# Kernel optimization log

Measured on AMD Instinct MI355X. Metric: run time of the kernel, lower is better.

## Reference

```python
import jax, jax.numpy as jnp
import numpy as np

B, S, D, H = 2, 2048, 512, 8
DK = D // H

def setup_inputs() -> dict:
    key = jax.random.key(0)
    ks = jax.random.split(key, 13)
    inp = {
        'query': jax.random.normal(ks[0], (B, S, D), jnp.float32),
        'key': jax.random.normal(ks[1], (B, S, D), jnp.float32),
        'value': jax.random.normal(ks[2], (B, S, D), jnp.float32),
        'group_prob': jax.random.uniform(ks[3], (B, S, S), jnp.float32),
        'mask': jax.random.randint(ks[4], (B, S, S), 0, 2, jnp.int32),
        'Wq': jax.random.normal(ks[5], (D, D), jnp.float32) * 0.02,
        'bq': jax.random.normal(ks[6], (D,), jnp.float32) * 0.02,
        'Wk': jax.random.normal(ks[7], (D, D), jnp.float32) * 0.02,
        'bk': jax.random.normal(ks[8], (D,), jnp.float32) * 0.02,
        'Wv': jax.random.normal(ks[9], (D, D), jnp.float32) * 0.02,
        'bv': jax.random.normal(ks[10], (D,), jnp.float32) * 0.02,
        'Wo': jax.random.normal(ks[11], (D, D), jnp.float32) * 0.02,
        'bo': jax.random.normal(ks[12], (D,), jnp.float32) * 0.02,
    }
    return inp

def reference(query, key, value, group_prob, mask, Wq, bq, Wk, bk, Wv, bv, Wo, bo):
    # project and split heads: [B,S,D] -> [B,H,S,dk]
    def proj(x, W, b):
        return (x @ W.T + b).reshape(B, S, H, DK).transpose(0, 2, 1, 3)
    q = proj(query, Wq, bq)
    k = proj(key, Wk, bk)
    v = proj(value, Wv, bv)
    scale = 1.0 / np.sqrt(DK).astype(np.float32)
    scores = jnp.einsum('bhqd,bhkd->bhqk', q, k) * scale  # [B,H,S,S]
    # allowed = mask | identity-diagonal; disallowed positions get -1e9
    diag = jnp.eye(S, dtype=bool)
    allowed = (mask.astype(bool) | diag)[:, None, :, :]  # [B,1,S,S]
    scores = jnp.where(allowed, scores, jnp.float32(-1e9))
    p_attn = jax.nn.softmax(scores, axis=-1) * group_prob[:, None, :, :]
    # dropout is identity in eval/deterministic mode
    x = jnp.einsum('bhqk,bhkd->bhqd', p_attn, v)  # [B,H,S,dk]
    x = x.transpose(0, 2, 1, 3).reshape(B, S, D)
    return x @ Wo.T + bo
```

## Files before the change

### kernel.cpp

```cpp
#include <hip/hip_runtime.h>
#include <hip/hip_bf16.h>
#include <cstdint>
#include <cstddef>

typedef __attribute__((ext_vector_type(8))) short bf16x8;
typedef __attribute__((ext_vector_type(4))) float f32x4;
typedef __attribute__((address_space(3))) void lds_void;
typedef const __attribute__((address_space(1))) void g_void;

constexpr int Bc = 2, Sc = 2048, Dc = 512, Hc = 8, DKc = 64;
constexpr int SPLIT = 2;
constexpr int NKT = Sc / 64;
constexpr int KT_PER = NKT / SPLIT;
constexpr float CSC = 0.18033688011112042f;

struct alignas(16) us8 { unsigned short u[8]; };
struct alignas(8) us4 { unsigned short u[4]; };

__device__ __forceinline__ unsigned short f2bf(float x) {
  union { float f; unsigned int u; } v; v.f = x;
  unsigned int r = (v.u + 0x7FFFu + ((v.u >> 16) & 1u)) >> 16;
  return (unsigned short)r;
}

__device__ __forceinline__ float bf2f(unsigned short u) {
  union { unsigned int u; float f; } v; v.u = ((unsigned int)u) << 16;
  return v.f;
}

__device__ __forceinline__ us8 cvt8(float4 a, float4 b) {
  us8 o;
  o.u[0] = f2bf(a.x); o.u[1] = f2bf(a.y); o.u[2] = f2bf(a.z); o.u[3] = f2bf(a.w);
  o.u[4] = f2bf(b.x); o.u[5] = f2bf(b.y); o.u[6] = f2bf(b.z); o.u[7] = f2bf(b.w);
  return o;
}

struct PArgs {
  const float* g; const int* m; unsigned short* gp;
  const float* wsrc[4]; unsigned short* wdst[4];
};

__global__ __launch_bounds__(256)
void prepass(PArgs pa)
{
  const int bx = blockIdx.x;
  const int tid = threadIdx.x;
  if (bx < 2048) {
    const int idx = bx;
    const int b = idx >> 10, rest = idx & 1023, qt = rest >> 5, kt = rest & 31;
    const int colb = tid & 15, hi = (tid >> 4) & 3, wid = tid >> 6;
    const int q = qt * 64 + wid * 16 + colb;
    const int k0 = kt * 64 + hi * 4;
    const float* grow = pa.g + ((size_t)b * Sc + q) * Sc + k0;
    const int* mrow = pa.m + ((size_t)b * Sc + q) * Sc + k0;
    unsigned short vals[16];
#pragma unroll
    for (int n = 0; n < 4; ++n) {
      float4 gv = *(const float4*)(grow + n * 16);
      int4 mv = *(const int4*)(mrow + n * 16);
      const int kb = k0 + n * 16;
      const float gg[4] = {gv.x, gv.y, gv.z, gv.w};
      const int mm[4] = {mv.x, mv.y, mv.z, mv.w};
#pragma unroll
      for (int rr = 0; rr < 4; ++rr) {
        const bool allowed = (mm[rr] != 0) || (kb + rr == q);
        vals[n * 4 + rr] = allowed ? (unsigned short)(f2bf(gg[rr]) | 1u) : (unsigned short)0;
      }
    }
    us8* o = (us8*)(pa.gp + (((size_t)idx * 256) + tid) * 16);
    o[0] = *(us8*)&vals[0];
    o[1] = *(us8*)&vals[8];
  } else {
    const int r = bx - 2048;
    const int wi = r >> 3, sub = r & 7;
    const float* s = pa.wsrc[wi];
    unsigned short* d = pa.wdst[wi];
#pragma unroll
    for (int t = 0; t < 16; ++t) {
      const int i = sub * 4096 + t * 256 + tid;
      float4 a = ((const float4*)s)[(size_t)i * 2];
      float4 b = ((const float4*)s)[(size_t)i * 2 + 1];
      ((us8*)d)[i] = cvt8(a, b);
    }
  }
}

struct GArgs {
  const void* A[3];
  const unsigned short* W[3];
  const float* bias[3];
  void* C[3];
  int mode[3];
  float osc[3];
};

template<int A_FP32>
__global__ __launch_bounds__(256)
void gemm_bn64(GArgs ga)
{
  __shared__ unsigned short As[128][64];
  __shared__ unsigned short Bs[64][64];

  constexpr int K = 512, N = 512;
  const int z = blockIdx.z;
  const unsigned short* Wp = ga.W[z];
  const float* bias = ga.bias[z];
  const int mode = ga.mode[z];
  const float osc = ga.osc[z];

  const int tid = threadIdx.x, lane = tid & 63, w = tid >> 6;
  const int m0 = blockIdx.x * 128, n0 = blockIdx.y * 64;
  const int wm = w >> 1, wn = w & 1;
  const int colb = lane & 15, hi = lane >> 4, rowb = hi * 4;
  const int swz = (colb & 7) << 4;

  f32x4 acc[4][2];
#pragma unroll
  for (int i = 0; i < 4; ++i)
#pragma unroll
    for (int j = 0; j < 2; ++j) acc[i][j] = (f32x4){0.f, 0.f, 0.f, 0.f};

  const int lrow8 = lane >> 3;
  const int cb = ((lane & 7) * 16) ^ (lrow8 << 4);

  for (int k0 = 0; k0 < K; k0 += 64) {
    if (k0) __syncthreads();
#pragma unroll
    for (int i = 0; i < 2; ++i) {
      const int u = w + i * 4;
      const int row = u * 8 + lrow8;
      const unsigned short* bsrc = Wp + (size_t)(n0 + row) * K + k0 + (cb >> 1);
      __builtin_amdgcn_global_load_lds((g_void*)bsrc, (lds_void*)((char*)&Bs[0][0] + u * 1024), 16, 0, 0);
    }
    if (A_FP32) {
      const float* Af = (const float*)ga.A[z];
#pragma unroll
      for (int i = 0; i < 4; ++i) {
        const int u = w * 4 + i;
        const int row = u * 8 + lrow8;
        const float* src = Af + (size_t)(m0 + row) * K + k0 + (cb >> 1);
        float4 v0 = *(const float4*)src, v1 = *(const float4*)(src + 4);
        *(us8*)((char*)&As[0][0] + u * 1024 + lane * 16) = cvt8(v0, v1);
      }
    } else {
      const unsigned short* Ab = (const unsigned short*)ga.A[z];
#pragma unroll
      for (int i = 0; i < 4; ++i) {
        const int u = w * 4 + i;
        const int row = u * 8 + lrow8;
        const unsigned short* asrc = Ab + (size_t)(m0 + row) * K + k0 + (cb >> 1);
        __builtin_amdgcn_global_load_lds((g_void*)asrc, (lds_void*)((char*)&As[0][0] + u * 1024), 16, 0, 0);
      }
    }
    asm volatile("s_waitcnt vmcnt(0)" ::: "memory");
    __syncthreads();

    char* ab = (char*)&As[0][0];
    char* bb = (char*)&Bs[0][0];
#pragma unroll
    for (int kk = 0; kk < 2; ++kk) {
      bf16x8 af[4], bfr[2];
#pragma unroll
      for (int mf = 0; mf < 4; ++mf) {
        const int ar = wm * 64 + mf * 16 + colb;
        af[mf] = *(const bf16x8*)(ab + ar * 128 + ((kk * 64 + hi * 16) ^ swz));
      }
#pragma unroll
      for (int nf = 0; nf < 2; ++nf) {
        const int br = wn * 32 + nf * 16 + colb;
        bfr[nf] = *(const bf16x8*)(bb + br * 128 + ((kk * 64 + hi * 16) ^ swz));
      }
      __builtin_amdgcn_s_setprio(1);
#pragma unroll
      for (int mf = 0; mf < 4; ++mf)
#pragma unroll
        for (int nf = 0; nf < 2; ++nf)
          acc[mf][nf] = __builtin_amdgcn_mfma_f32_16x16x32_bf16(af[mf], bfr[nf], acc[mf][nf], 0, 0, 0);
      __builtin_amdgcn_s_setprio(0);
    }
  }

#pragma unroll
  for (int nf = 0; nf < 2; ++nf) {
    const int gn = n0 + wn * 32 + nf * 16 + colb;
    const float bv = bias[gn];
    if (mode == 1) {
      unsigned short* Cp = (unsigned short*)ga.C[z];
#pragma unroll
      for (int mf = 0; mf < 4; ++mf) {
        const int gm = m0 + wm * 64 + mf * 16 + rowb;
        const int bb_ = gm >> 11, ss = gm & (Sc - 1);
        us4 vv;
#pragma unroll
        for (int rr = 0; rr < 4; ++rr) vv.u[rr] = f2bf(acc[mf][nf][rr] + bv);
        *(us4*)(Cp + ((size_t)bb_ * N + gn) * Sc + ss) = vv;
      }
    } else if (mode == 0) {
      unsigned short* Cp = (unsigned short*)ga.C[z];
#pragma unroll
      for (int mf = 0; mf < 4; ++mf)
#pragma unroll
        for (int rr = 0; rr < 4; ++rr) {
          const int gm = m0 + wm * 64 + mf * 16 + rowb + rr;
          Cp[(size_t)gm * N + gn] = f2bf((acc[mf][nf][rr] + bv) * osc);
        }
    } else {
      float* Cp = (float*)ga.C[z];
#pragma unroll
      for (int mf = 0; mf < 4; ++mf)
#pragma unroll
        for (int rr = 0; rr < 4; ++rr) {
          const int gm = m0 + wm * 64 + mf * 16 + rowb + rr;
          Cp[(size_t)gm * N + gn] = acc[mf][nf][rr] + bv;
        }
    }
  }
}

__global__ __launch_bounds__(256, 4)
void attn_split(const unsigned short* __restrict__ Qb,
                const unsigned short* __restrict__ Kb,
                const unsigned short* __restrict__ Vt,
                const unsigned short* __restrict__ Gp,
                float* __restrict__ Pacc,
                float* __restrict__ Pml)
{
  __shared__ unsigned short Ks[2][64][64];
  __shared__ unsigned short Vs[2][64][64];
  __shared__ unsigned short Ps[4][16][64];

  const int tid = threadIdx.x, lane = tid & 63, wid = tid >> 6;
  const int bh = blockIdx.x, b = bh >> 3, h = bh & 7;
  const int qt = blockIdx.y, q0 = qt * 64;
  const int sp = blockIdx.z;
  const int kt0 = sp * KT_PER;

  const int colb = lane & 15;
  const int hi = lane >> 4;
  const int rowb = hi * 4;
  const int c3s = (colb & 7) << 4;

  bf16x8 qf[2];
  {
    const unsigned short* qp = Qb + ((size_t)(b * Sc + q0 + wid * 16 + colb) * Dc + h * DKc + hi * 8);
    qf[0] = *(const bf16x8*)qp;
    qf[1] = *(const bf16x8*)(qp + 32);
  }

  f32x4 acc[4] = {{0,0,0,0},{0,0,0,0},{0,0,0,0},{0,0,0,0}};
  float mrun = -1e30f, lrun = 0.f;

  auto stageKV = [&](int bufI, int kt) {
    const int k0 = kt * 64;
#pragma unroll
    for (int i = 0; i < 2; ++i) {
      const int obase = wid * 1024 + i * 4096;
      const int row = (obase >> 7) + (lane >> 3);
      const int cb = ((lane & 7) * 16) ^ ((row & 7) << 4);
      const unsigned short* ksrc = Kb + (size_t)(b * Sc + k0 + row) * Dc + h * DKc + (cb >> 1);
      const unsigned short* vsrc = Vt + ((size_t)b * Dc + h * DKc + row) * Sc + k0 + (cb >> 1);
      __builtin_amdgcn_global_load_lds((g_void*)ksrc, (lds_void*)((char*)&Ks[bufI][0][0] + obase), 16, 0, 0);
      __builtin_amdgcn_global_load_lds((g_void*)vsrc, (lds_void*)((char*)&Vs[bufI][0][0] + obase), 16, 0, 0);
    }
  };

  const unsigned short* gtile = Gp + (((size_t)(b * 1024 + qt * 32)) * 256 + tid) * 16;
  us8 gcur0, gcur1;
  auto loadG = [&](int kt, us8& g0, us8& g1) {
    const us8* p = (const us8*)(gtile + (size_t)kt * 4096);
    g0 = p[0]; g1 = p[1];
  };

  stageKV(0, kt0);
  loadG(kt0, gcur0, gcur1);
  asm volatile("s_waitcnt vmcnt(0)" ::: "memory");
  __syncthreads();

  int buf = 0;
  char* psbase = (char*)&Ps[wid][0][0];

  for (int j = 0; j < KT_PER; ++j) {
    const int kt = kt0 + j;
    us8 gn0, gn1;
    if (j + 1 < KT_PER) {
      stageKV(buf ^ 1, kt + 1);
      loadG(kt + 1, gn0, gn1);
    }

    f32x4 sf[4] = {{0,0,0,0},{0,0,0,0},{0,0,0,0},{0,0,0,0}};
    char* ksb = (char*)&Ks[buf][0][0];
    __builtin_amdgcn_s_setprio(1);
#pragma unroll
    for (int kk = 0; kk < 2; ++kk) {
#pragma unroll
      for (int n = 0; n < 4; ++n) {
        const int krow = n * 16 + colb;
        bf16x8 kf = *(const bf16x8*)(ksb + krow * 128 + ((kk * 64 + hi * 16) ^ ((krow & 7) << 4)));
        sf[n] = __builtin_amdgcn_mfma_f32_16x16x32_bf16(kf, qf[kk], sf[n], 0, 0, 0);
      }
    }
    __builtin_amdgcn_s_setprio(0);

    float tm = sf[0][0];
#pragma unroll
    for (int n = 0; n < 4; ++n)
#pragma unroll
      for (int rr = 0; rr < 4; ++rr) tm = fmaxf(tm, sf[n][rr]);
    tm = fmaxf(tm, __shfl_xor(tm, 16));
    tm = fmaxf(tm, __shfl_xor(tm, 32));

    if (__any(tm > mrun + 8.f)) {
      const float mnew = fmaxf(mrun, tm);
      const float alpha = __builtin_amdgcn_exp2f(mrun - mnew);
      mrun = mnew;
#pragma unroll
      for (int n = 0; n < 4; ++n)
#pragma unroll
        for (int rr = 0; rr < 4; ++rr) acc[n][rr] *= alpha;
      lrun *= alpha;
    }

    float rsum = 0.f;
    unsigned int pw[8];
#pragma unroll
    for (int n = 0; n < 4; ++n) {
#pragma unroll
      for (int s2 = 0; s2 < 2; ++s2) {
        const int jv = n * 4 + s2 * 2;
        const unsigned short u0 = (jv < 8) ? gcur0.u[jv] : gcur1.u[jv - 8];
        const unsigned short u1 = (jv + 1 < 8) ? gcur0.u[jv + 1] : gcur1.u[jv + 1 - 8];
        const float p0 = __builtin_amdgcn_exp2f(sf[n][s2 * 2]     - mrun);
        const float p1 = __builtin_amdgcn_exp2f(sf[n][s2 * 2 + 1] - mrun);
        rsum = fmaf(p0, (float)(u0 & 1u), rsum);
        rsum = fmaf(p1, (float)(u1 & 1u), rsum);
        const float q0v = p0 * bf2f(u0), q1v = p1 * bf2f(u1);
        asm("v_cvt_pk_bf16_f32 %0, %1, %2" : "=v"(pw[n * 2 + s2]) : "v"(q0v), "v"(q1v));
      }
    }
    rsum += __shfl_xor(rsum, 16);
    rsum += __shfl_xor(rsum, 32);
    lrun += rsum;

#pragma unroll
    for (int n = 0; n < 4; ++n) {
      const unsigned long long w64 = ((unsigned long long)pw[n * 2 + 1] << 32) | pw[n * 2];
      *(unsigned long long*)(psbase + colb * 128 + ((n * 32 + hi * 8) ^ c3s)) = w64;
    }

    char* vsb = (char*)&Vs[buf][0][0];
    __builtin_amdgcn_s_setprio(1);
#pragma unroll
    for (int kk = 0; kk < 2; ++kk) {
      bf16x8 pf = *(const bf16x8*)(psbase + colb * 128 + ((kk * 64 + hi * 16) ^ c3s));
#pragma unroll
      for (int n = 0; n < 4; ++n) {
        const int vrow = n * 16 + colb;
        bf16x8 vf = *(const bf16x8*)(vsb + vrow * 128 + ((kk * 64 + hi * 16) ^ ((vrow & 7) << 4)));
        acc[n] = __builtin_amdgcn_mfma_f32_16x16x32_bf16(vf, pf, acc[n], 0, 0, 0);
      }
    }
    __builtin_amdgcn_s_setprio(0);

    asm volatile("s_waitcnt vmcnt(0)" ::: "memory");
    __syncthreads();
    buf ^= 1;
    if (j + 1 < KT_PER) { gcur0 = gn0; gcur1 = gn1; }
  }

  const size_t blin = ((size_t)bh * 32 + qt) * SPLIT + sp;
  float* pa = Pacc + blin * 4096;
#pragma unroll
  for (int n = 0; n < 4; ++n)
#pragma unroll
    for (int rr = 0; rr < 4; ++rr)
      pa[(size_t)(n * 16 + rowb + rr) * 64 + wid * 16 + colb] = acc[n][rr];
  if (hi == 0) {
    float* pm = Pml + blin * 128;
    pm[wid * 16 + colb] = mrun;
    pm[64 + wid * 16 + colb] = lrun;
  }
}

__global__ __launch_bounds__(256)
void attn_reduce(const float* __restrict__ Pacc, const float* __restrict__ Pml,
                 unsigned short* __restrict__ Xb)
{
  const int gidx = blockIdx.x;
  const int bh = gidx >> 5, qt = gidx & 31;
  const int b = bh >> 3, h = bh & 7;
  const int tid = threadIdx.x;
  const int qi = tid & 63;
  const int d0 = (tid >> 6) * 16;
  const size_t pb = (size_t)gidx * SPLIT;

  float m[SPLIT], l[SPLIT];
  float mstar = -3.0e38f;
#pragma unroll
  for (int s = 0; s < SPLIT; ++s) {
    m[s] = Pml[(pb + s) * 128 + qi];
    l[s] = Pml[(pb + s) * 128 + 64 + qi];
    mstar = fmaxf(mstar, m[s]);
  }
  float w[SPLIT], denom = 0.f;
#pragma unroll
  for (int s = 0; s < SPLIT; ++s) { w[s] = __builtin_amdgcn_exp2f(m[s] - mstar); denom += w[s] * l[s]; }
  const float inv = 1.0f / denom;

  unsigned short vals[16];
#pragma unroll
  for (int j = 0; j < 16; ++j) {
    float a = 0.f;
#pragma unroll
    for (int s = 0; s < SPLIT; ++s)
      a += w[s] * Pacc[(pb + s) * 4096 + (size_t)(d0 + j) * 64 + qi];
    vals[j] = f2bf(a * inv);
  }
  unsigned short* xp = Xb + ((size_t)(b * Sc) + qt * 64 + qi) * Dc + h * DKc + d0;
  *(us8*)xp = *(us8*)&vals[0];
  *(us8*)(xp + 8) = *(us8*)&vals[8];
}

extern "C" void kernel_launch(void* const* d_in, const int* in_sizes, int n_in,
                              void* d_out, int out_size, void* d_ws, size_t ws_size,
                              hipStream_t stream)
{
  const float* query = (const float*)d_in[0];
  const float* key_  = (const float*)d_in[1];
  const float* value = (const float*)d_in[2];
  const float* gprob = (const float*)d_in[3];
  const int*   mask  = (const int*)d_in[4];
  const float* Wq = (const float*)d_in[5];
  const float* bq = (const float*)d_in[6];
  const float* Wk = (const float*)d_in[7];
  const float* bk = (const float*)d_in[8];
  const float* Wv = (const float*)d_in[9];
  const float* bv = (const float*)d_in[10];
  const float* Wo = (const float*)d_in[11];
  const float* bo = (const float*)d_in[12];
  float* out = (float*)d_out;

  const size_t elems = (size_t)Bc * Sc * Dc;
  const size_t gelems = (size_t)Bc * Sc * Sc;
  const size_t welems = (size_t)Dc * Dc;

  char* base = (char*)d_ws;
  unsigned short* Qb = (unsigned short*)(base);
  unsigned short* Kb = Qb + elems;
  unsigned short* Vt = Kb + elems;
  unsigned short* Xb = Vt + elems;
  unsigned short* Gp = Xb + elems;
  unsigned short* Wqb = Gp + gelems;
  unsigned short* Wkb = Wqb + welems;
  unsigned short* Wvb = Wkb + welems;
  unsigned short* Wob = Wvb + welems;
  float* Pacc = (float*)(Wob + welems);
  float* Pml  = Pacc + (size_t)(Bc * Hc) * 32 * SPLIT * 4096;

  PArgs pa;
  pa.g = gprob; pa.m = mask; pa.gp = Gp;
  pa.wsrc[0] = Wq; pa.wdst[0] = Wqb;
  pa.wsrc[1] = Wk; pa.wdst[1] = Wkb;
  pa.wsrc[2] = Wv; pa.wdst[2] = Wvb;
  pa.wsrc[3] = Wo; pa.wdst[3] = Wob;
  hipLaunchKernelGGL(prepass, dim3(2080), dim3(256), 0, stream, pa);

  GArgs gq;
  gq.A[0] = (const void*)query; gq.W[0] = Wqb; gq.bias[0] = bq; gq.C[0] = (void*)Qb; gq.mode[0] = 0; gq.osc[0] = CSC;
  gq.A[1] = (const void*)key_;  gq.W[1] = Wkb; gq.bias[1] = bk; gq.C[1] = (void*)Kb; gq.mode[1] = 0; gq.osc[1] = 1.0f;
  gq.A[2] = (const void*)value; gq.W[2] = Wvb; gq.bias[2] = bv; gq.C[2] = (void*)Vt; gq.mode[2] = 1; gq.osc[2] = 1.0f;
  hipLaunchKernelGGL((gemm_bn64<1>), dim3(32, 8, 3), dim3(256), 0, stream, gq);

  dim3 ga(Bc * Hc, Sc / 64, SPLIT);
  hipLaunchKernelGGL(attn_split, ga, dim3(256), 0, stream, Qb, Kb, Vt, Gp, Pacc, Pml);
  hipLaunchKernelGGL(attn_reduce, dim3(Bc * Hc * 32), dim3(256), 0, stream, Pacc, Pml, Xb);

  GArgs go;
  go.A[0] = (const void*)Xb; go.W[0] = Wob; go.bias[0] = bo; go.C[0] = (void*)out; go.mode[0] = 2; go.osc[0] = 1.0f;
  go.A[1] = go.A[0]; go.W[1] = go.W[0]; go.bias[1] = go.bias[0]; go.C[1] = go.C[0]; go.mode[1] = 2; go.osc[1] = 1.0f;
  go.A[2] = go.A[0]; go.W[2] = go.W[0]; go.bias[2] = go.bias[0]; go.C[2] = go.C[0]; go.mode[2] = 2; go.osc[2] = 1.0f;
  hipLaunchKernelGGL((gemm_bn64<0>), dim3(32, 8, 1), dim3(256), 0, stream, go);
}
```

Baseline: 101.3 us.

## Shrink attention KV tile to 32 and raise split-K to four

Halves the key/value tile per iteration from 64 to 32 and doubles the number of key splits from 2 to 4, so the attention grid has twice as many blocks. The launch-bounds occupancy hint goes from 4 to 8 blocks per SIMD set. The shared-memory K/V/P buffers, swizzles and MFMA loops are rewritten for the narrower tile, and the prepass that packs group_prob and the mask is re-laid out to 32-wide tiles to match. The aim is more parallelism and latency hiding through smaller per-block LDS and register footprint. In exchange there are more barriers per unit of work and more partial results for the reduce kernel to combine.

Result: slower. 117.1 us (+15.6%).

```diff
diff --git a/kernel.cpp b/kernel.cpp
--- a/kernel.cpp
+++ b/kernel.cpp
@@ -9,8 +9,9 @@
 typedef const __attribute__((address_space(1))) void g_void;
 
 constexpr int Bc = 2, Sc = 2048, Dc = 512, Hc = 8, DKc = 64;
-constexpr int SPLIT = 2;
-constexpr int NKT = Sc / 64;
+constexpr int SPLIT = 4;
+constexpr int KVB = 32;
+constexpr int NKT = Sc / KVB;
 constexpr int KT_PER = NKT / SPLIT;
 constexpr float CSC = 0.18033688011112042f;
 
@@ -45,33 +46,31 @@
 {
   const int bx = blockIdx.x;
   const int tid = threadIdx.x;
-  if (bx < 2048) {
+  if (bx < 4096) {
     const int idx = bx;
-    const int b = idx >> 10, rest = idx & 1023, qt = rest >> 5, kt = rest & 31;
+    const int b = idx >> 11, rest = idx & 2047, qt = rest >> 6, kt = rest & 63;
     const int colb = tid & 15, hi = (tid >> 4) & 3, wid = tid >> 6;
     const int q = qt * 64 + wid * 16 + colb;
-    const int k0 = kt * 64 + hi * 4;
-    const float* grow = pa.g + ((size_t)b * Sc + q) * Sc + k0;
-    const int* mrow = pa.m + ((size_t)b * Sc + q) * Sc + k0;
-    unsigned short vals[16];
-#pragma unroll
-    for (int n = 0; n < 4; ++n) {
+    const int kb = kt * KVB + hi * 4;
+    const float* grow = pa.g + ((size_t)b * Sc + q) * Sc + kb;
+    const int* mrow = pa.m + ((size_t)b * Sc + q) * Sc + kb;
+    unsigned short vals[8];
+#pragma unroll
+    for (int n = 0; n < 2; ++n) {
       float4 gv = *(const float4*)(grow + n * 16);
       int4 mv = *(const int4*)(mrow + n * 16);
-      const int kb = k0 + n * 16;
+      const int kbase = kb + n * 16;
       const float gg[4] = {gv.x, gv.y, gv.z, gv.w};
       const int mm[4] = {mv.x, mv.y, mv.z, mv.w};
 #pragma unroll
       for (int rr = 0; rr < 4; ++rr) {
-        const bool allowed = (mm[rr] != 0) || (kb + rr == q);
+        const bool allowed = (mm[rr] != 0) || (kbase + rr == q);
         vals[n * 4 + rr] = allowed ? (unsigned short)(f2bf(gg[rr]) | 1u) : (unsigned short)0;
       }
     }
-    us8* o = (us8*)(pa.gp + (((size_t)idx * 256) + tid) * 16);
-    o[0] = *(us8*)&vals[0];
-    o[1] = *(us8*)&vals[8];
+    *(us8*)(pa.gp + (((size_t)idx * 256) + tid) * 8) = *(us8*)&vals[0];
   } else {
-    const int r = bx - 2048;
+    const int r = bx - 4096;
     const int wi = r >> 3, sub = r & 7;
     const float* s = pa.wsrc[wi];
     unsigned short* d = pa.wdst[wi];
@@ -217,7 +216,7 @@
   }
 }
 
-__global__ __launch_bounds__(256, 4)
+__global__ __launch_bounds__(256, 8)
 void attn_split(const unsigned short* __restrict__ Qb,
                 const unsigned short* __restrict__ Kb,
                 const unsigned short* __restrict__ Vt,
@@ -225,9 +224,9 @@
                 float* __restrict__ Pacc,
                 float* __restrict__ Pml)
 {
-  __shared__ unsigned short Ks[2][64][64];
-  __shared__ unsigned short Vs[2][64][64];
-  __shared__ unsigned short Ps[4][16][64];
+  __shared__ unsigned short Ks[2][32][64];
+  __shared__ unsigned short Vs[2][64][32];
+  __shared__ unsigned short Ps[4][16][32];
 
   const int tid = threadIdx.x, lane = tid & 63, wid = tid >> 6;
   const int bh = blockIdx.x, b = bh >> 3, h = bh & 7;
@@ -238,7 +237,7 @@
   const int colb = lane & 15;
   const int hi = lane >> 4;
   const int rowb = hi * 4;
-  const int c3s = (colb & 7) << 4;
+  const int c2s = (colb & 3) << 4;
 
   bf16x8 qf[2];
   {
@@ -251,28 +250,29 @@
   float mrun = -1e30f, lrun = 0.f;
 
   auto stageKV = [&](int bufI, int kt) {
-    const int k0 = kt * 64;
-#pragma unroll
-    for (int i = 0; i < 2; ++i) {
-      const int obase = wid * 1024 + i * 4096;
-      const int row = (obase >> 7) + (lane >> 3);
+    const int k0 = kt * KVB;
+    {
+      const int row = wid * 8 + (lane >> 3);
       const int cb = ((lane & 7) * 16) ^ ((row & 7) << 4);
       const unsigned short* ksrc = Kb + (size_t)(b * Sc + k0 + row) * Dc + h * DKc + (cb >> 1);
+      __builtin_amdgcn_global_load_lds((g_void*)ksrc, (lds_void*)((char*)&Ks[bufI][0][0] + wid * 1024), 16, 0, 0);
+    }
+    {
+      const int row = wid * 16 + (lane >> 2);
+      const int cb = ((lane & 3) * 16) ^ ((row & 3) << 4);
       const unsigned short* vsrc = Vt + ((size_t)b * Dc + h * DKc + row) * Sc + k0 + (cb >> 1);
-      __builtin_amdgcn_global_load_lds((g_void*)ksrc, (lds_void*)((char*)&Ks[bufI][0][0] + obase), 16, 0, 0);
-      __builtin_amdgcn_global_load_lds((g_void*)vsrc, (lds_void*)((char*)&Vs[bufI][0][0] + obase), 16, 0, 0);
+      __builtin_amdgcn_global_load_lds((g_void*)vsrc, (lds_void*)((char*)&Vs[bufI][0][0] + wid * 1024), 16, 0, 0);
     }
   };
 
-  const unsigned short* gtile = Gp + (((size_t)(b * 1024 + qt * 32)) * 256 + tid) * 16;
-  us8 gcur0, gcur1;
-  auto loadG = [&](int kt, us8& g0, us8& g1) {
-    const us8* p = (const us8*)(gtile + (size_t)kt * 4096);
-    g0 = p[0]; g1 = p[1];
+  const unsigned short* gtile = Gp + (((size_t)(b * 2048 + qt * 64)) * 256 + tid) * 8;
+  us8 gcur;
+  auto loadG = [&](int kt, us8& g0) {
+    g0 = *(const us8*)(gtile + (size_t)kt * 2048);
   };
 
   stageKV(0, kt0);
-  loadG(kt0, gcur0, gcur1);
+  loadG(kt0, gcur);
   asm volatile("s_waitcnt vmcnt(0)" ::: "memory");
   __syncthreads();
 
@@ -281,19 +281,19 @@
 
   for (int j = 0; j < KT_PER; ++j) {
     const int kt = kt0 + j;
-    us8 gn0, gn1;
+    us8 gn0;
     if (j + 1 < KT_PER) {
       stageKV(buf ^ 1, kt + 1);
-      loadG(kt + 1, gn0, gn1);
-    }
-
-    f32x4 sf[4] = {{0,0,0,0},{0,0,0,0},{0,0,0,0},{0,0,0,0}};
+      loadG(kt + 1, gn0);
+    }
+
+    f32x4 sf[2] = {{0,0,0,0},{0,0,0,0}};
     char* ksb = (char*)&Ks[buf][0][0];
     __builtin_amdgcn_s_setprio(1);
 #pragma unroll
     for (int kk = 0; kk < 2; ++kk) {
 #pragma unroll
-      for (int n = 0; n < 4; ++n) {
+      for (int n = 0; n < 2; ++n) {
         const int krow = n * 16 + colb;
         bf16x8 kf = *(const bf16x8*)(ksb + krow * 128 + ((kk * 64 + hi * 16) ^ ((krow & 7) << 4)));
         sf[n] = __builtin_amdgcn_mfma_f32_16x16x32_bf16(kf, qf[kk], sf[n], 0, 0, 0);
@@ -301,11 +301,8 @@
     }
     __builtin_amdgcn_s_setprio(0);
 
-    float tm = sf[0][0];
-#pragma unroll
-    for (int n = 0; n < 4; ++n)
-#pragma unroll
-      for (int rr = 0; rr < 4; ++rr) tm = fmaxf(tm, sf[n][rr]);
+    float tm = fmaxf(fmaxf(fmaxf(sf[0][0], sf[0][1]), fmaxf(sf[0][2], sf[0][3])),
+                     fmaxf(fmaxf(sf[1][0], sf[1][1]), fmaxf(sf[1][2], sf[1][3])));
     tm = fmaxf(tm, __shfl_xor(tm, 16));
     tm = fmaxf(tm, __shfl_xor(tm, 32));
 
@@ -321,14 +318,14 @@
     }
 
     float rsum = 0.f;
-    unsigned int pw[8];
-#pragma unroll
-    for (int n = 0; n < 4; ++n) {
+    unsigned int pw[4];
+#pragma unroll
+    for (int n = 0; n < 2; ++n) {
 #pragma unroll
       for (int s2 = 0; s2 < 2; ++s2) {
         const int jv = n * 4 + s2 * 2;
-        const unsigned short u0 = (jv < 8) ? gcur0.u[jv] : gcur1.u[jv - 8];
-        const unsigned short u1 = (jv + 1 < 8) ? gcur0.u[jv + 1] : gcur1.u[jv + 1 - 8];
+        const unsigned short u0 = gcur.u[jv];
+        const unsigned short u1 = gcur.u[jv + 1];
         const float p0 = __builtin_amdgcn_exp2f(sf[n][s2 * 2]     - mrun);
         const float p1 = __builtin_amdgcn_exp2f(sf[n][s2 * 2 + 1] - mrun);
         rsum = fmaf(p0, (float)(u0 & 1u), rsum);
@@ -342,29 +339,26 @@
     lrun += rsum;
 
 #pragma unroll
+    for (int n = 0; n < 2; ++n) {
+      const unsigned long long w64 = ((unsigned long long)pw[n * 2 + 1] << 32) | pw[n * 2];
+      *(unsigned long long*)(psbase + colb * 64 + ((n * 32 + hi * 8) ^ c2s)) = w64;
+    }
+
+    char* vsb = (char*)&Vs[buf][0][0];
+    bf16x8 pf = *(const bf16x8*)(psbase + colb * 64 + ((hi * 16) ^ c2s));
+    __builtin_amdgcn_s_setprio(1);
+#pragma unroll
     for (int n = 0; n < 4; ++n) {
-      const unsigned long long w64 = ((unsigned long long)pw[n * 2 + 1] << 32) | pw[n * 2];
-      *(unsigned long long*)(psbase + colb * 128 + ((n * 32 + hi * 8) ^ c3s)) = w64;
-    }
-
-    char* vsb = (char*)&Vs[buf][0][0];
-    __builtin_amdgcn_s_setprio(1);
-#pragma unroll
-    for (int kk = 0; kk < 2; ++kk) {
-      bf16x8 pf = *(const bf16x8*)(psbase + colb * 128 + ((kk * 64 + hi * 16) ^ c3s));
-#pragma unroll
-      for (int n = 0; n < 4; ++n) {
-        const int vrow = n * 16 + colb;
-        bf16x8 vf = *(const bf16x8*)(vsb + vrow * 128 + ((kk * 64 + hi * 16) ^ ((vrow & 7) << 4)));
-        acc[n] = __builtin_amdgcn_mfma_f32_16x16x32_bf16(vf, pf, acc[n], 0, 0, 0);
-      }
+      const int vrow = n * 16 + colb;
+      bf16x8 vf = *(const bf16x8*)(vsb + vrow * 64 + ((hi * 16) ^ ((vrow & 3) << 4)));
+      acc[n] = __builtin_amdgcn_mfma_f32_16x16x32_bf16(vf, pf, acc[n], 0, 0, 0);
     }
     __builtin_amdgcn_s_setprio(0);
 
     asm volatile("s_waitcnt vmcnt(0)" ::: "memory");
     __syncthreads();
     buf ^= 1;
-    if (j + 1 < KT_PER) { gcur0 = gn0; gcur1 = gn1; }
+    if (j + 1 < KT_PER) gcur = gn0;
   }
 
   const size_t blin = ((size_t)bh * 32 + qt) * SPLIT + sp;
@@ -462,7 +456,7 @@
   pa.wsrc[1] = Wk; pa.wdst[1] = Wkb;
   pa.wsrc[2] = Wv; pa.wdst[2] = Wvb;
   pa.wsrc[3] = Wo; pa.wdst[3] = Wob;
-  hipLaunchKernelGGL(prepass, dim3(2080), dim3(256), 0, stream, pa);
+  hipLaunchKernelGGL(prepass, dim3(4128), dim3(256), 0, stream, pa);
 
   GArgs gq;
   gq.A[0] = (const void*)query; gq.W[0] = Wqb; gq.bias[0] = bq; gq.C[0] = (void*)Qb; gq.mode[0] = 0; gq.osc[0] = CSC;
```
